# Kernel optimization log

Measured on AMD Instinct MI355X. Metric: run time of the kernel, lower is better.

The kernel has to match this reference:

```python
import jax, jax.numpy as jnp
import numpy as np

NV, NE, NT = 20000, 40000, 30000
D, H, L = 512, 8, 2
HD = D // H
SCALE = float(np.sqrt(HD))
EV, EE, ET = 160000, 160000, 120000
LN_EPS = 1e-5


def _layer_norm(x, g, b):
    m = jnp.mean(x, axis=-1, keepdims=True)
    v = jnp.mean((x - m) ** 2, axis=-1, keepdims=True)
    return (x - m) * jax.lax.rsqrt(v + LN_EPS) * g + b


def _attn_layer(x, ei, W, b, g, bt):
    # x: [N, D]; ei: [2, E]; W: [4, D, D] (q,k,v,out); b: [4, D]
    n = x.shape[0]
    resid = x
    q = (x @ W[0] + b[0]).reshape(n, H, HD)
    k = (x @ W[1] + b[1]).reshape(n, H, HD)
    v = (x @ W[2] + b[2]).reshape(n, H, HD)
    src, dst = ei[0], ei[1]
    # per-edge scores: query at target, key at source (k[edge_index[1]] gather in original)
    scores = jnp.sum(q[dst] * k[src], axis=-1) / SCALE        # [E, H]
    # NOTE: original applies softmax over dim=0, i.e. globally over the edge axis
    w = jax.nn.softmax(scores, axis=0)                         # [E, H]
    msgs = w[:, :, None] * v[src]                              # [E, H, HD]
    out = jax.ops.segment_sum(msgs, dst, num_segments=n)      # [N, H, HD]
    out = out.reshape(n, D) @ W[3] + b[3]
    return _layer_norm(out + resid, g, bt)


def _attn_stack(x, ei, W, b, g, bt):
    for l in range(L):
        x = _attn_layer(x, ei, W[l], b[l], g[l], bt[l])
    return x


def setup_inputs() -> dict:
    key = jax.random.key(0)
    ks = jax.random.split(key, 16)
    inp = {}
    inp['vertices'] = jax.random.normal(ks[0], (NV, D), jnp.float32)
    inp['edge_features'] = jax.random.normal(ks[1], (NE, D), jnp.float32)
    inp['triangle_features'] = jax.random.normal(ks[2], (NT, D), jnp.float32)
    inp['v_embed'] = jax.random.normal(ks[3], (NV, D), jnp.float32)
    inp['e_embed'] = jax.random.normal(ks[4], (NE, D), jnp.float32)
    inp['t_embed'] = jax.random.normal(ks[5], (NT, D), jnp.float32)
    inp['v_pos'] = jax.random.normal(ks[6], (NV, D), jnp.float32) * 0.1
    inp['e_pos'] = jax.random.normal(ks[7], (NE, D), jnp.float32) * 0.1
    inp['t_pos'] = jax.random.normal(ks[8], (NT, D), jnp.float32) * 0.1
    for name, k2 in (('v', ks[9]), ('e', ks[10]), ('t', ks[11])):
        inp[name + 'W'] = jax.random.normal(k2, (L, 4, D, D), jnp.float32) * 0.02
        inp[name + 'B'] = jnp.zeros((L, 4, D), jnp.float32)
        inp[name + 'G'] = jnp.ones((L, D), jnp.float32)
        inp[name + 'Bt'] = jnp.zeros((L, D), jnp.float32)
    inp['head_W'] = jax.random.normal(ks[12], (3, D, D), jnp.float32) * 0.02
    inp['head_b'] = jnp.zeros((3, D), jnp.float32)
    inp['v_ei'] = jax.random.randint(ks[13], (2, EV), 0, NV, jnp.int32)
    inp['e_ei'] = jax.random.randint(ks[14], (2, EE), 0, NE, jnp.int32)
    inp['t_ei'] = jax.random.randint(ks[15], (2, ET), 0, NT, jnp.int32)
    return inp


def reference(vertices, edge_features, triangle_features, v_embed, e_embed, t_embed,
              v_pos, e_pos, t_pos, vW, vB, vG, vBt, eW, eB, eG, eBt,
              tW, tB, tG, tBt, head_W, head_b, v_ei, e_ei, t_ei):
    # embedding(arange(N)) == full table lookup; add positional params and input features
    v = v_embed + v_pos + vertices
    e = e_embed + e_pos + edge_features
    t = t_embed + t_pos + triangle_features
    v = _attn_stack(v, v_ei, vW, vB, vG, vBt)
    e = _attn_stack(e, e_ei, eW, eB, eG, eBt)
    t = _attn_stack(t, t_ei, tW, tB, tG, tBt)
    v_out = v @ head_W[0] + head_b[0]
    e_out = e @ head_W[1] + head_b[1]
    t_out = t @ head_W[2] + head_b[2]
    return (v_out, e_out, t_out)
```

## Files before the change

### kernel.cpp

```cpp
#include <hip/hip_runtime.h>


typedef __attribute__((ext_vector_type(8))) __bf16 bf16x8;
typedef __attribute__((ext_vector_type(4))) float f32x4;
typedef __attribute__((ext_vector_type(8))) unsigned short ushort8v;
typedef __attribute__((ext_vector_type(4))) unsigned short ushort4v;

__device__ __forceinline__ float b2f(unsigned short u) {
  union { unsigned u; float f; } x; x.u = (unsigned)u << 16; return x.f;
}
__device__ __forceinline__ unsigned short f2b(float f) {
  union { float f; unsigned u; } x; x.f = f;
  unsigned r = x.u + 0x7fffu + ((x.u >> 16) & 1u);
  return (unsigned short)(r >> 16);
}
__device__ __forceinline__ int xcd_swizzle(int orig, int nwg) {
  const int xcd = orig & 7, lin = orig >> 3;
  const int q = nwg >> 3, r8 = nwg & 7;
  return (xcd < r8 ? xcd * (q + 1) : r8 * (q + 1) + (xcd - r8) * q) + lin;
}
__device__ __forceinline__ void stage16(const void* g, void* lds_uniform) {
  __builtin_amdgcn_global_load_lds(
      (const __attribute__((address_space(1))) void*)g,
      (__attribute__((address_space(3))) void*)lds_uniform, 16, 0, 0);
}

struct IB {
  const float4* a[3]; const float4* b[3]; const float4* c[3];
  unsigned short* xb[3];
  long long cum[4];
};
struct HB {
  const int* ei[3]; int E[3]; int cum[4];
  int* deg[3]; const int* rowptr[3]; int* srcs[3];
};
struct PB {
  const int* deg[3]; int* rowptr[3]; int N[3]; int nbcum[4];
};
struct GB {
  const unsigned short* A[3]; const unsigned short* BT[3];
  const float* bias[3]; void* C[3];
  int M[3]; int cum[4];
};
struct SB {
  const unsigned short* qkv[3]; const int* srcs[3]; const int* rowptr[3];
  float* sc[3]; float* pm[3]; float* ps[3];
  int N[3]; int cum[4];
};
struct MB {
  const float* pm[3]; const float* ps[3]; int nslots[3];
};
struct AB {
  const unsigned short* qkv[3]; const float* sc[3]; const int* srcs[3];
  const int* rowptr[3]; unsigned short* agg[3];
  int N[3]; int cum[4];
};
struct LB {
  const unsigned short* proj[3]; const float* g[3]; const float* bt[3];
  unsigned short* xb[3]; int N[3]; int cum[4];
};
__device__ __forceinline__ int find3(int b, const int* cum) {
  return (b >= cum[1]) + (b >= cum[2]);
}

__global__ __launch_bounds__(256) void init_b_kernel(IB ib)
{
  long long total = ib.cum[3];
  long long stride = (long long)gridDim.x * 256;
  for (long long i = (long long)blockIdx.x * 256 + threadIdx.x; i < total; i += stride) {
    int s = (i >= ib.cum[1]) + (i >= ib.cum[2]);
    long long j = i - ib.cum[s];
    float4 av = ib.a[s][j], bv = ib.b[s][j], cv = ib.c[s][j];
    ushort4v o;
    o.x = f2b(av.x + bv.x + cv.x); o.y = f2b(av.y + bv.y + cv.y);
    o.z = f2b(av.z + bv.z + cv.z); o.w = f2b(av.w + bv.w + cv.w);
    *(ushort4v*)(ib.xb[s] + j * 4) = o;
  }
}

__global__ __launch_bounds__(256) void transpose_all_kernel(
    const float* W0, const float* W1, const float* W2, const float* Wh,
    unsigned short* WT)
{
  __shared__ float t[32][33];
  int z = blockIdx.z;
  const float* src = (z < 8)  ? W0 + (size_t)z * 262144
                   : (z < 16) ? W1 + (size_t)(z - 8) * 262144
                   : (z < 24) ? W2 + (size_t)(z - 16) * 262144
                              : Wh + (size_t)(z - 24) * 262144;
  unsigned short* dst = WT + (size_t)z * 262144;
  int bx = blockIdx.x * 32, by = blockIdx.y * 32;
  int tx = threadIdx.x, ty = threadIdx.y;
  #pragma unroll
  for (int i = 0; i < 32; i += 8)
    t[ty + i][tx] = src[(size_t)(by + ty + i) * 512 + bx + tx];
  __syncthreads();
  #pragma unroll
  for (int i = 0; i < 32; i += 8) {
    int c = bx + ty + i;
    int p = (c & ~0x3C) | ((c & 0x30) >> 2) | ((c & 0x0C) << 2);
    dst[(size_t)p * 512 + by + tx] = f2b(t[tx][ty + i]);
  }
}

template<int OUT_BF16>
__global__ __launch_bounds__(512, 2) void gemm_big_kernel(GB gb, int Ncols)
{
  constexpr int K = 512;
  __shared__ unsigned short smem[81920];

  const int b = blockIdx.x;
  const int s = find3(b, gb.cum);
  const int wgid = xcd_swizzle(b - gb.cum[s], gb.cum[s + 1] - gb.cum[s]);
  const unsigned short* A  = gb.A[s];
  const unsigned short* BT = gb.BT[s];
  const float* bias = gb.bias[s];
  const int M = gb.M[s];

  const int tiles_n = Ncols >> 8;
  const int tm = wgid / tiles_n;
  const int tn = wgid - tm * tiles_n;
  const int row0 = tm << 8, col0 = tn << 8;
  const int lane = threadIdx.x & 63, wid = threadIdx.x >> 6;
  const int wr = (wid >> 2) << 7;
  const int wc = (wid & 3) << 6;

  f32x4 acc[8][4];
  #pragma unroll
  for (int i = 0; i < 8; ++i)
    #pragma unroll
    for (int j = 0; j < 4; ++j) acc[i][j] = (f32x4)0.f;

  int srow[4], scsw[4], sseg[4];
  #pragma unroll
  for (int i = 0; i < 4; ++i) {
    int seg = (i << 3) | wid;
    int idx = (seg << 6) | lane;
    int row = idx >> 3, ch = idx & 7;
    sseg[i] = seg; srow[i] = row; scsw[i] = ch ^ (row & 7);
  }

  #define STG_A(buf3, kb_, i)                                                 \
    { int ra = row0 + srow[i]; ra = (ra < M) ? ra : (M - 1);                  \
      stage16(A + (size_t)ra * K + (kb_) + (scsw[i] << 3),                    \
              smem + (buf3) * 16384 + (sseg[i] << 9)); }
  #define STG_B(buf2, kb_, i)                                                 \
    { int rb = col0 + srow[i];                                                \
      stage16(BT + (size_t)rb * K + (kb_) + (scsw[i] << 3),                   \
              smem + 49152 + (buf2) * 16384 + (sseg[i] << 9)); }

  STG_B(0, 0, 0) STG_B(0, 0, 1) STG_B(0, 0, 2) STG_B(0, 0, 3)
  STG_A(0, 0, 0) STG_A(0, 0, 1) STG_A(0, 0, 2) STG_A(0, 0, 3)
  STG_A(1, 64, 0) STG_A(1, 64, 1) STG_A(1, 64, 2) STG_A(1, 64, 3)
  asm volatile("s_waitcnt vmcnt(4)" ::: "memory");
  __builtin_amdgcn_s_barrier();

  const int lm = lane & 15;
  const int kbl = (lane >> 4) << 4;

  #pragma unroll
  for (int kt = 0; kt < 8; ++kt) {
    const char* Asb = (const char*)(smem + (kt % 3) * 16384);
    const char* Bsb = (const char*)(smem + 49152 + (kt & 1) * 16384);
    const int kb1 = (kt + 1) << 6, kb2 = (kt + 2) << 6;

    auto rdA = [&](int mi, int kk) -> bf16x8 {
      int r = wr + (mi << 4) + lm;
      int kb = (kk << 6) + kbl;
      return *(const bf16x8*)(Asb + (r << 7) + (kb ^ ((r & 7) << 4)));
    };
    auto rdB = [&](int ni, int kk) -> bf16x8 {
      int r = wc + (ni << 4) + lm;
      int kb = (kk << 6) + kbl;
      return *(const bf16x8*)(Bsb + (r << 7) + (kb ^ ((r & 7) << 4)));
    };

    bf16x8 av[4], bv[4];

    #pragma unroll
    for (int i = 0; i < 4; ++i) { av[i] = rdA(i, 0); bv[i] = rdB(i, 0); }
    if (kt < 7) {
      STG_B((kt + 1) & 1, kb1, 0) STG_B((kt + 1) & 1, kb1, 1)
      STG_B((kt + 1) & 1, kb1, 2) STG_B((kt + 1) & 1, kb1, 3)
    }
    __builtin_amdgcn_s_barrier();
    __builtin_amdgcn_s_setprio(1);
    #pragma unroll
    for (int mi = 0; mi < 4; ++mi)
      #pragma unroll
      for (int ni = 0; ni < 4; ++ni)
        acc[mi][ni] = __builtin_amdgcn_mfma_f32_16x16x32_bf16(
            bv[ni], av[mi], acc[mi][ni], 0, 0, 0);
    __builtin_amdgcn_s_setprio(0);
    __builtin_amdgcn_s_barrier();

    #pragma unroll
    for (int i = 0; i < 4; ++i) av[i] = rdA(4 + i, 0);
    if (kt < 6) {
      STG_A((kt + 2) % 3, kb2, 0) STG_A((kt + 2) % 3, kb2, 1)
      STG_A((kt + 2) % 3, kb2, 2) STG_A((kt + 2) % 3, kb2, 3)
    }
    __builtin_amdgcn_s_barrier();
    __builtin_amdgcn_s_setprio(1);
    #pragma unroll
    for (int mi = 0; mi < 4; ++mi)
      #pragma unroll
      for (int ni = 0; ni < 4; ++ni)
        acc[4 + mi][ni] = __builtin_amdgcn_mfma_f32_16x16x32_bf16(
            bv[ni], av[mi], acc[4 + mi][ni], 0, 0, 0);
    __builtin_amdgcn_s_setprio(0);
    __builtin_amdgcn_s_barrier();

    #pragma unroll
    for (int i = 0; i < 4; ++i) { av[i] = rdA(i, 1); bv[i] = rdB(i, 1); }
    __builtin_amdgcn_s_barrier();
    __builtin_amdgcn_s_setprio(1);
    #pragma unroll
    for (int mi = 0; mi < 4; ++mi)
      #pragma unroll
      for (int ni = 0; ni < 4; ++ni)
        acc[mi][ni] = __builtin_amdgcn_mfma_f32_16x16x32_bf16(
            bv[ni], av[mi], acc[mi][ni], 0, 0, 0);
    __builtin_amdgcn_s_setprio(0);
    __builtin_amdgcn_s_barrier();

    #pragma unroll
    for (int i = 0; i < 4; ++i) av[i] = rdA(4 + i, 1);
    __builtin_amdgcn_s_barrier();
    __builtin_amdgcn_s_setprio(1);
    #pragma unroll
    for (int mi = 0; mi < 4; ++mi)
      #pragma unroll
      for (int ni = 0; ni < 4; ++ni)
        acc[4 + mi][ni] = __builtin_amdgcn_mfma_f32_16x16x32_bf16(
            bv[ni], av[mi], acc[4 + mi][ni], 0, 0, 0);
    __builtin_amdgcn_s_setprio(0);

    if (kt < 6) {
      asm volatile("s_waitcnt vmcnt(4) lgkmcnt(0)" ::: "memory");
      __builtin_amdgcn_s_barrier();
    } else if (kt == 6) {
      asm volatile("s_waitcnt vmcnt(0) lgkmcnt(0)" ::: "memory");
      __builtin_amdgcn_s_barrier();
    }
  }
  #undef STG_A
  #undef STG_B

  const int mrow = lane & 15;
  const int t4 = (lane >> 4) << 4;
  float bsv[16];
  #pragma unroll
  for (int ni = 0; ni < 4; ++ni) {
    float4 bvv = *(const float4*)(bias + col0 + wc + t4 + (ni << 2));
    bsv[4*ni+0] = bvv.x; bsv[4*ni+1] = bvv.y; bsv[4*ni+2] = bvv.z; bsv[4*ni+3] = bvv.w;
  }

  if (OUT_BF16) {
    unsigned short* C = (unsigned short*)gb.C[s];
    #pragma unroll
    for (int mi = 0; mi < 8; ++mi) {
      int rowg = row0 + wr + (mi << 4) + mrow;
      if (rowg < M) {
        ushort8v o0, o1;
        #pragma unroll
        for (int r = 0; r < 4; ++r) {
          o0[r]     = f2b(acc[mi][0][r] + bsv[r]);
          o0[4 + r] = f2b(acc[mi][1][r] + bsv[4 + r]);
          o1[r]     = f2b(acc[mi][2][r] + bsv[8 + r]);
          o1[4 + r] = f2b(acc[mi][3][r] + bsv[12 + r]);
        }
        unsigned short* cp = C + (size_t)rowg * Ncols + col0 + wc + t4;
        *(ushort8v*)cp = o0;
        *(ushort8v*)(cp + 8) = o1;
      }
    }
  } else {
    float* C = (float*)gb.C[s];
    #pragma unroll
    for (int mi = 0; mi < 8; ++mi) {
      int rowg = row0 + wr + (mi << 4) + mrow;
      if (rowg < M) {
        float* cp = C + (size_t)rowg * Ncols + col0 + wc + t4;
        #pragma unroll
        for (int ni = 0; ni < 4; ++ni) {
          float4 v;
          v.x = acc[mi][ni][0] + bsv[4*ni+0];
          v.y = acc[mi][ni][1] + bsv[4*ni+1];
          v.z = acc[mi][ni][2] + bsv[4*ni+2];
          v.w = acc[mi][ni][3] + bsv[4*ni+3];
          *(float4*)(cp + (ni << 2)) = v;
        }
      }
    }
  }
}

template<int OUT_BF16>
__global__ __launch_bounds__(256) void gemm_sm_kernel(GB gb, int Ncols)
{
  constexpr int K = 512;
  __shared__ unsigned short As[8192];
  __shared__ unsigned short Bs[8192];

  const int b = blockIdx.x;
  const int s = find3(b, gb.cum);
  const int wgid = xcd_swizzle(b - gb.cum[s], gb.cum[s + 1] - gb.cum[s]);
  const unsigned short* A  = gb.A[s];
  const unsigned short* BT = gb.BT[s];
  const float* bias = gb.bias[s];
  const int M = gb.M[s];

  const int tiles_n = Ncols >> 7;
  const int tm = wgid / tiles_n;
  const int tn = wgid - tm * tiles_n;
  const int row0 = tm << 7, col0 = tn << 7;
  const int lane = threadIdx.x & 63, wid = threadIdx.x >> 6;
  const int wm = (wid >> 1) << 6, wn = (wid & 1) << 6;

  f32x4 acc[4][4];
  #pragma unroll
  for (int i = 0; i < 4; ++i)
    #pragma unroll
    for (int j = 0; j < 4; ++j) acc[i][j] = (f32x4)0.f;

  int srow[4], scsw[4], sseg[4];
  #pragma unroll
  for (int i = 0; i < 4; ++i) {
    int seg = (i << 2) | wid;
    int idx = (seg << 6) | lane;
    int row = idx >> 3, ch = idx & 7;
    sseg[i] = seg; srow[i] = row; scsw[i] = ch ^ (row & 7);
  }

  #pragma unroll
  for (int kt = 0; kt < 8; ++kt) {
    const int kbase = kt << 6;
    #pragma unroll
    for (int i = 0; i < 4; ++i) {
      int ra = row0 + srow[i]; ra = (ra < M) ? ra : (M - 1);
      stage16(A + (size_t)ra * K + kbase + (scsw[i] << 3), As + (sseg[i] << 9));
      int rb = col0 + srow[i];
      stage16(BT + (size_t)rb * K + kbase + (scsw[i] << 3), Bs + (sseg[i] << 9));
    }
    asm volatile("s_waitcnt vmcnt(0)" ::: "memory");
    __syncthreads();

    #pragma unroll
    for (int kk = 0; kk < 2; ++kk) {
      const int kb = (kk << 6) + ((lane >> 4) << 4);
      bf16x8 af[4], bfr[4];
      #pragma unroll
      for (int mi = 0; mi < 4; ++mi) {
        int r = wm + (mi << 4) + (lane & 15);
        af[mi] = *(const bf16x8*)((const char*)As + (r << 7) + (kb ^ ((r & 7) << 4)));
      }
      #pragma unroll
      for (int ni = 0; ni < 4; ++ni) {
        int r = wn + (ni << 4) + (lane & 15);
        bfr[ni] = *(const bf16x8*)((const char*)Bs + (r << 7) + (kb ^ ((r & 7) << 4)));
      }
      #pragma unroll
      for (int mi = 0; mi < 4; ++mi)
        #pragma unroll
        for (int ni = 0; ni < 4; ++ni)
          acc[mi][ni] = __builtin_amdgcn_mfma_f32_16x16x32_bf16(
              bfr[ni], af[mi], acc[mi][ni], 0, 0, 0);
    }
    __syncthreads();
  }

  const int mrow = lane & 15;
  const int t4 = (lane >> 4) << 4;
  float bsv[16];
  #pragma unroll
  for (int ni = 0; ni < 4; ++ni) {
    float4 bvv = *(const float4*)(bias + col0 + wn + t4 + (ni << 2));
    bsv[4*ni+0] = bvv.x; bsv[4*ni+1] = bvv.y; bsv[4*ni+2] = bvv.z; bsv[4*ni+3] = bvv.w;
  }

  if (OUT_BF16) {
    unsigned short* C = (unsigned short*)gb.C[s];
    #pragma unroll
    for (int mi = 0; mi < 4; ++mi) {
      int rowg = row0 + wm + (mi << 4) + mrow;
      if (rowg < M) {
        ushort8v o0, o1;
        #pragma unroll
        for (int r = 0; r < 4; ++r) {
          o0[r]     = f2b(acc[mi][0][r] + bsv[r]);
          o0[4 + r] = f2b(acc[mi][1][r] + bsv[4 + r]);
          o1[r]     = f2b(acc[mi][2][r] + bsv[8 + r]);
          o1[4 + r] = f2b(acc[mi][3][r] + bsv[12 + r]);
        }
        unsigned short* cp = C + (size_t)rowg * Ncols + col0 + wn + t4;
        *(ushort8v*)cp = o0;
        *(ushort8v*)(cp + 8) = o1;
      }
    }
  } else {
    float* C = (float*)gb.C[s];
    #pragma unroll
    for (int mi = 0; mi < 4; ++mi) {
      int rowg = row0 + wm + (mi << 4) + mrow;
      if (rowg < M) {
        float* cp = C + (size_t)rowg * Ncols + col0 + wn + t4;
        #pragma unroll
        for (int ni = 0; ni < 4; ++ni) {
          float4 v;
          v.x = acc[mi][ni][0] + bsv[4*ni+0];
          v.y = acc[mi][ni][1] + bsv[4*ni+1];
          v.z = acc[mi][ni][2] + bsv[4*ni+2];
          v.w = acc[mi][ni][3] + bsv[4*ni+3];
          *(float4*)(cp + (ni << 2)) = v;
        }
      }
    }
  }
}

__global__ __launch_bounds__(256) void scores_b_kernel(SB sb)
{
  int b = blockIdx.x;
  int s = find3(b, sb.cum);
  int lb = b - sb.cum[s];
  const unsigned short* qkv = sb.qkv[s];
  const int* srcs = sb.srcs[s];
  float* sc = sb.sc[s];
  int wid = threadIdx.x >> 6, lane = threadIdx.x & 63;
  int n = (lb << 2) | wid;
  float mx = -1e30f, sm = 0.f;
  if (n < sb.N[s]) {
    int beg = sb.rowptr[s][n], end = sb.rowptr[s][n + 1];
    if (beg < end) {
      ushort8v qv = *(const ushort8v*)(qkv + (size_t)n * 1536 + (lane << 3));
      float qf[8];
      #pragma unroll
      for (int j = 0; j < 8; ++j) qf[j] = b2f(qv[j]);
      int i = beg;
      for (; i + 2 <= end; i += 2) {
        int s0 = srcs[i], s1 = srcs[i + 1];
        ushort8v k0 = *(const ushort8v*)(qkv + (size_t)s0 * 1536 + 512 + (lane << 3));
        ushort8v k1 = *(const ushort8v*)(qkv + (size_t)s1 * 1536 + 512 + (lane << 3));
        float p0 = 0.f, p1 = 0.f;
        #pragma unroll
        for (int j = 0; j < 8; ++j) { p0 += qf[j] * b2f(k0[j]); p1 += qf[j] * b2f(k1[j]); }
        p0 += __shfl_xor(p0, 1); p1 += __shfl_xor(p1, 1);
        p0 += __shfl_xor(p0, 2); p1 += __shfl_xor(p1, 2);
        p0 += __shfl_xor(p0, 4); p1 += __shfl_xor(p1, 4);
        p0 *= 0.125f; p1 *= 0.125f;
        float nm = fmaxf(mx, fmaxf(p0, p1));
        sm = sm * __expf(mx - nm) + __expf(p0 - nm) + __expf(p1 - nm);
        mx = nm;
        if (!(lane & 7)) {
          sc[(size_t)i * 8 + (lane >> 3)] = p0;
          sc[(size_t)(i + 1) * 8 + (lane >> 3)] = p1;
        }
      }
      if (i < end) {
        int s0 = srcs[i];
        ushort8v k0 = *(const ushort8v*)(qkv + (size_t)s0 * 1536 + 512 + (lane << 3));
        float p0 = 0.f;
        #pragma unroll
        for (int j = 0; j < 8; ++j) p0 += qf[j] * b2f(k0[j]);
        p0 += __shfl_xor(p0, 1);
        p0 += __shfl_xor(p0, 2);
        p0 += __shfl_xor(p0, 4);
        p0 *= 0.125f;
        float nm = fmaxf(mx, p0);
        sm = sm * __expf(mx - nm) + __expf(p0 - nm);
        mx = nm;
        if (!(lane & 7)) sc[(size_t)i * 8 + (lane >> 3)] = p0;
      }
    }
  }
  if (!(lane & 7)) {
    size_t slot = ((size_t)lb << 2) | wid;
    sb.pm[s][slot * 8 + (lane >> 3)] = mx;
    sb.ps[s][slot * 8 + (lane >> 3)] = sm;
  }
}

__device__ __forceinline__ void pair_reduce_block(
    float (&m)[8], float (&s)[8], float* redm, float* reds)
{
  int lane = threadIdx.x & 63, wid = threadIdx.x >> 6;
  #pragma unroll
  for (int h = 0; h < 8; ++h)
    #pragma unroll
    for (int off = 1; off < 64; off <<= 1) {
      float om = __shfl_xor(m[h], off);
      float os = __shfl_xor(s[h], off);
      float M = fmaxf(m[h], om);
      s[h] = s[h] * __expf(m[h] - M) + os * __expf(om - M);
      m[h] = M;
    }
  if (lane == 0) {
    #pragma unroll
    for (int h = 0; h < 8; ++h) { redm[h * 4 + wid] = m[h]; reds[h * 4 + wid] = s[h]; }
  }
  __syncthreads();
  if (threadIdx.x == 0) {
    #pragma unroll
    for (int h = 0; h < 8; ++h) {
      float M = redm[h * 4], S = reds[h * 4];
      #pragma unroll
      for (int w = 1; w < 4; ++w) {
        float om = redm[h * 4 + w], os = reds[h * 4 + w];
        float nM = fmaxf(M, om);
        S = S * __expf(M - nM) + os * __expf(om - nM);
        M = nM;
      }
      m[h] = M; s[h] = S;
    }
  }
}

__global__ __launch_bounds__(256) void gms_part_b_kernel(
    MB mb, float* pm2, float* ps2)
{
  __shared__ float redm[32], reds[32];
  int s = blockIdx.x >> 8, j = blockIdx.x & 255;
  const float* pm = mb.pm[s];
  const float* ps = mb.ps[s];
  float m[8], sv[8];
  #pragma unroll
  for (int h = 0; h < 8; ++h) { m[h] = -1e30f; sv[h] = 0.f; }
  for (int i = j * 256 + threadIdx.x; i < mb.nslots[s]; i += 65536) {
    #pragma unroll
    for (int h = 0; h < 8; ++h) {
      float mi = pm[(size_t)i * 8 + h], si = ps[(size_t)i * 8 + h];
      float M = fmaxf(m[h], mi);
      sv[h] = sv[h] * __expf(m[h] - M) + si * __expf(mi - M);
      m[h] = M;
    }
  }
  pair_reduce_block(m, sv, redm, reds);
  if (threadIdx.x == 0) {
    #pragma unroll
    for (int h = 0; h < 8; ++h) {
      pm2[(s * 256 + j) * 8 + h] = m[h];
      ps2[(s * 256 + j) * 8 + h] = sv[h];
    }
  }
}

__global__ __launch_bounds__(256) void gms_final_b_kernel(
    const float* pm2, const float* ps2, float* gmax, float* ginv)
{
  __shared__ float redm[32], reds[32];
  int s = blockIdx.x;
  float m[8], sv[8];
  #pragma unroll
  for (int h = 0; h < 8; ++h) {
    m[h]  = pm2[(s * 256 + threadIdx.x) * 8 + h];
    sv[h] = ps2[(s * 256 + threadIdx.x) * 8 + h];
  }
  pair_reduce_block(m, sv, redm, reds);
  if (threadIdx.x == 0) {
    #pragma unroll
    for (int h = 0; h < 8; ++h) { gmax[s * 8 + h] = m[h]; ginv[s * 8 + h] = 1.0f / sv[h]; }
  }
}

__global__ __launch_bounds__(256) void hist_b_kernel(HB hb)
{
  int b = blockIdx.x;
  int s = find3(b, hb.cum);
  int e = (b - hb.cum[s]) * 256 + threadIdx.x;
  if (e < hb.E[s]) atomicAdd(&hb.deg[s][hb.ei[s][hb.E[s] + e]], 1);
}

__global__ __launch_bounds__(1024) void scan_part_b_kernel(PB pb, int* bsums)
{
  __shared__ int wsum[16];
  int b = blockIdx.x;
  int s = (b >= pb.nbcum[1]) + (b >= pb.nbcum[2]);
  int lb = b - pb.nbcum[s];
  int i = lb * 1024 + threadIdx.x;
  int lane = threadIdx.x & 63, wid = threadIdx.x >> 6;
  int sv = (i < pb.N[s]) ? pb.deg[s][i] : 0;
  #pragma unroll
  for (int off = 1; off < 64; off <<= 1) {
    int t = __shfl_up(sv, off);
    if (lane >= off) sv += t;
  }
  if (lane == 63) wsum[wid] = sv;
  __syncthreads();
  if (threadIdx.x < 16) {
    int ws = wsum[threadIdx.x];
    #pragma unroll
    for (int off = 1; off < 16; off <<= 1) {
      int t = __shfl_up(ws, off);
      if (threadIdx.x >= off) ws += t;
    }
    wsum[threadIdx.x] = ws;
  }
  __syncthreads();
  if (wid > 0) sv += wsum[wid - 1];
  if (i < pb.N[s]) pb.rowptr[s][i + 1] = sv;
  if (threadIdx.x == 1023) bsums[s * 64 + lb] = sv;
}

__global__ __launch_bounds__(64) void scan_bsums_b_kernel(
    int* bsums, int nb0, int nb1, int nb2)
{
  int s = blockIdx.x;
  int nb = (s == 0) ? nb0 : (s == 1) ? nb1 : nb2;
  int* bs = bsums + s * 64;
  int lane = threadIdx.x;
  int v = (lane < nb) ? bs[lane] : 0;
  #pragma unroll
  for (int off = 1; off < 64; off <<= 1) {
    int t = __shfl_up(v, off);
    if (lane >= off) v += t;
  }
  int ex = __shfl_up(v, 1);
  if (lane == 0) ex = 0;
  if (lane < nb) bs[lane] = ex;
}

__global__ __launch_bounds__(1024) void scan_add_b_kernel(
    PB pb, const int* bsums)
{
  int b = blockIdx.x;
  int s = (b >= pb.nbcum[1]) + (b >= pb.nbcum[2]);
  int lb = b - pb.nbcum[s];
  int i = lb * 1024 + threadIdx.x;
  if (lb == 0 && threadIdx.x == 0) pb.rowptr[s][0] = 0;
  if (i < pb.N[s] && lb > 0) pb.rowptr[s][i + 1] += bsums[s * 64 + lb];
}

__global__ __launch_bounds__(256) void scatter_b_kernel(HB hb)
{
  int b = blockIdx.x;
  int s = find3(b, hb.cum);
  int e = (b - hb.cum[s]) * 256 + threadIdx.x;
  if (e < hb.E[s]) {
    const int* ei = hb.ei[s];
    int dst = ei[hb.E[s] + e];
    int pos = atomicAdd(&hb.deg[s][dst], 1);
    hb.srcs[s][hb.rowptr[s][dst] + pos] = ei[e];
  }
}

__global__ __launch_bounds__(256) void aggregate_b_kernel(
    AB ab, const float* gmaxg, const float* ginvg)
{
  int b = blockIdx.x;
  int s = find3(b, ab.cum);
  int lb = b - ab.cum[s];
  int wid = threadIdx.x >> 6, lane = threadIdx.x & 63;
  int n = (lb << 2) | wid;
  if (n >= ab.N[s]) return;
  const unsigned short* qkv = ab.qkv[s];
  const float* sc = ab.sc[s];
  const int* srcs = ab.srcs[s];
  int beg = ab.rowptr[s][n], end = ab.rowptr[s][n + 1];
  int h = lane >> 3;
  float gm  = gmaxg[s * 8 + h];
  float inv = ginvg[s * 8 + h];
  float acc[8] = {0.f,0.f,0.f,0.f,0.f,0.f,0.f,0.f};
  int i = beg;
  for (; i + 4 <= end; i += 4) {
    int s0 = srcs[i], s1 = srcs[i + 1], s2 = srcs[i + 2], s3 = srcs[i + 3];
    float w0 = __expf(sc[(size_t)i * 8 + h] - gm) * inv;
    float w1 = __expf(sc[(size_t)(i + 1) * 8 + h] - gm) * inv;
    float w2 = __expf(sc[(size_t)(i + 2) * 8 + h] - gm) * inv;
    float w3 = __expf(sc[(size_t)(i + 3) * 8 + h] - gm) * inv;
    ushort8v v0 = *(const ushort8v*)(qkv + (size_t)s0 * 1536 + 1024 + (lane << 3));
    ushort8v v1 = *(const ushort8v*)(qkv + (size_t)s1 * 1536 + 1024 + (lane << 3));
    ushort8v v2 = *(const ushort8v*)(qkv + (size_t)s2 * 1536 + 1024 + (lane << 3));
    ushort8v v3 = *(const ushort8v*)(qkv + (size_t)s3 * 1536 + 1024 + (lane << 3));
    #pragma unroll
    for (int j = 0; j < 8; ++j)
      acc[j] += (w0 * b2f(v0[j]) + w1 * b2f(v1[j]))
              + (w2 * b2f(v2[j]) + w3 * b2f(v3[j]));
  }
  for (; i < end; ++i) {
    int s0 = srcs[i];
    float w0 = __expf(sc[(size_t)i * 8 + h] - gm) * inv;
    ushort8v v0 = *(const ushort8v*)(qkv + (size_t)s0 * 1536 + 1024 + (lane << 3));
    #pragma unroll
    for (int j = 0; j < 8; ++j) acc[j] += w0 * b2f(v0[j]);
  }
  ushort8v o;
  #pragma unroll
  for (int j = 0; j < 8; ++j) o[j] = f2b(acc[j]);
  *(ushort8v*)(ab.agg[s] + (size_t)n * 512 + (lane << 3)) = o;
}

__global__ __launch_bounds__(256) void ln_b_kernel(LB lb_)
{
  int b = blockIdx.x;
  int s = find3(b, lb_.cum);
  int lb = b - lb_.cum[s];
  int wid = threadIdx.x >> 6, lane = threadIdx.x & 63;
  int n = (lb << 2) | wid;
  if (n >= lb_.N[s]) return;
  size_t base = (size_t)n * 512 + (lane << 3);
  ushort8v pv = *(const ushort8v*)(lb_.proj[s] + base);
  ushort8v xv = *(const ushort8v*)(lb_.xb[s] + base);
  float y[8];
  #pragma unroll
  for (int j = 0; j < 8; ++j) y[j] = b2f(pv[j]) + b2f(xv[j]);
  float sum = 0.f;
  #pragma unroll
  for (int j = 0; j < 8; ++j) sum += y[j];
  #pragma unroll
  for (int off = 1; off < 64; off <<= 1) sum += __shfl_xor(sum, off);
  float mean = sum * (1.f / 512.f);
  float vs = 0.f;
  #pragma unroll
  for (int j = 0; j < 8; ++j) { float d = y[j] - mean; vs += d * d; }
  #pragma unroll
  for (int off = 1; off < 64; off <<= 1) vs += __shfl_xor(vs, off);
  float rstd = rsqrtf(vs * (1.f / 512.f) + 1e-5f);
  int gi = lane << 3;
  ushort8v ob;
  #pragma unroll
  for (int j = 0; j < 8; ++j)
    ob[j] = f2b((y[j] - mean) * rstd * lb_.g[s][gi + j] + lb_.bt[s][gi + j]);
  *(ushort8v*)(lb_.xb[s] + base) = ob;
}

extern "C" void kernel_launch(void* const* d_in, const int* in_sizes, int n_in,
                              void* d_out, int out_size, void* d_ws, size_t ws_size,
                              hipStream_t stream)
{
  (void)n_in; (void)out_size;
  const float* feat[3] = {(const float*)d_in[0], (const float*)d_in[1], (const float*)d_in[2]};
  const float* emb[3]  = {(const float*)d_in[3], (const float*)d_in[4], (const float*)d_in[5]};
  const float* pos[3]  = {(const float*)d_in[6], (const float*)d_in[7], (const float*)d_in[8]};
  const float* W[3]  = {(const float*)d_in[9],  (const float*)d_in[13], (const float*)d_in[17]};
  const float* Bb[3] = {(const float*)d_in[10], (const float*)d_in[14], (const float*)d_in[18]};
  const float* G[3]  = {(const float*)d_in[11], (const float*)d_in[15], (const float*)d_in[19]};
  const float* Bt[3] = {(const float*)d_in[12], (const float*)d_in[16], (const float*)d_in[20]};
  const float* headW = (const float*)d_in[21];
  const float* headB = (const float*)d_in[22];
  const int* ei[3] = {(const int*)d_in[23], (const int*)d_in[24], (const int*)d_in[25]};

  int Ns[3], Es[3];
  for (int s = 0; s < 3; ++s) { Ns[s] = in_sizes[s] / 512; Es[s] = in_sizes[23 + s] / 2; }

  long long Noff[4] = {0}, Eoff[4] = {0}, Roff[4] = {0}, Poff[4] = {0};
  for (int s = 0; s < 3; ++s) {
    Noff[s + 1] = Noff[s] + Ns[s];
    Eoff[s + 1] = Eoff[s] + Es[s];
    Roff[s + 1] = Roff[s] + Ns[s] + 1;
    Poff[s + 1] = Poff[s] + ((Ns[s] + 3) / 4) * 4;
  }

  char* base = (char*)d_ws;
  size_t off = 0;
  auto carve = [&](size_t bytes) -> char* {
    char* r = base + off;
    off += (bytes + 255) & ~(size_t)255;
    return r;
  };
  unsigned short* WT   = (unsigned short*)carve((size_t)27 * 262144 * 2);
  unsigned short* XB   = (unsigned short*)carve((size_t)Noff[3] * 512 * 2);
  unsigned short* QKV  = (unsigned short*)carve((size_t)Noff[3] * 1536 * 2);
  float*          SC   = (float*)carve((size_t)Eoff[3] * 8 * 4);
  unsigned short* AGG  = (unsigned short*)carve((size_t)Noff[3] * 512 * 2);
  int*   ROWPTR = (int*)carve((size_t)Roff[3] * 4);
  int*   DEG    = (int*)carve((size_t)Noff[3] * 4);
  int*   SRCS   = (int*)carve((size_t)Eoff[3] * 4);
  int*   BSUMS  = (int*)carve(3 * 64 * 4);
  float* PARTM  = (float*)carve((size_t)Poff[3] * 8 * 4);
  float* PARTS1 = (float*)carve((size_t)Poff[3] * 8 * 4);
  float* PARTM2 = (float*)carve(3 * 256 * 8 * 4);
  float* PARTS2 = (float*)carve(3 * 256 * 8 * 4);
  float* GMAX   = (float*)carve(256);
  float* GINV   = (float*)carve(256);
  if (off > ws_size) return;

  unsigned short* XBs[3];  unsigned short* QKVs[3]; float* SCs[3];
  unsigned short* AGGs[3]; int* ROWPTRs[3]; int* DEGs[3]; int* SRCSs[3];
  float* PMs[3]; float* PSs[3];
  for (int s = 0; s < 3; ++s) {
    XBs[s]  = XB  + Noff[s] * 512;
    QKVs[s] = QKV + Noff[s] * 1536;
    SCs[s]  = SC  + Eoff[s] * 8;
    AGGs[s] = AGG + Noff[s] * 512;
    ROWPTRs[s] = ROWPTR + Roff[s];
    DEGs[s] = DEG + Noff[s];
    SRCSs[s] = SRCS + Eoff[s];
    PMs[s] = PARTM + Poff[s] * 8;
    PSs[s] = PARTS1 + Poff[s] * 8;
  }

  transpose_all_kernel<<<dim3(16, 16, 27), dim3(32, 8), 0, stream>>>(
      W[0], W[1], W[2], headW, WT);

  IB ib;
  for (int s = 0; s < 3; ++s) {
    ib.a[s] = (const float4*)feat[s]; ib.b[s] = (const float4*)emb[s];
    ib.c[s] = (const float4*)pos[s];  ib.xb[s] = XBs[s];
  }
  ib.cum[0] = 0;
  for (int s = 0; s < 3; ++s) ib.cum[s + 1] = ib.cum[s] + (long long)Ns[s] * 128;
  init_b_kernel<<<2048, 256, 0, stream>>>(ib);

  HB hb;
  hb.cum[0] = 0;
  for (int s = 0; s < 3; ++s) {
    hb.ei[s] = ei[s]; hb.E[s] = Es[s];
    hb.cum[s + 1] = hb.cum[s] + (Es[s] + 255) / 256;
    hb.deg[s] = DEGs[s]; hb.rowptr[s] = ROWPTRs[s]; hb.srcs[s] = SRCSs[s];
  }
  PB pb;
  pb.nbcum[0] = 0;
  for (int s = 0; s < 3; ++s) {
    pb.deg[s] = DEGs[s]; pb.rowptr[s] = ROWPTRs[s]; pb.N[s] = Ns[s];
    pb.nbcum[s + 1] = pb.nbcum[s] + (Ns[s] + 1023) / 1024;
  }
  hipMemsetAsync(DEG, 0, (size_t)Noff[3] * 4, stream);
  hist_b_kernel<<<hb.cum[3], 256, 0, stream>>>(hb);
  scan_part_b_kernel<<<pb.nbcum[3], 1024, 0, stream>>>(pb, BSUMS);
  scan_bsums_b_kernel<<<3, 64, 0, stream>>>(
      BSUMS, (Ns[0] + 1023) / 1024, (Ns[1] + 1023) / 1024, (Ns[2] + 1023) / 1024);
  scan_add_b_kernel<<<pb.nbcum[3], 1024, 0, stream>>>(pb, BSUMS);
  hipMemsetAsync(DEG, 0, (size_t)Noff[3] * 4, stream);
  scatter_b_kernel<<<hb.cum[3], 256, 0, stream>>>(hb);

  int nsbcum[4] = {0}, mtcum[4] = {0}, mtscum[4] = {0};
  for (int s = 0; s < 3; ++s) {
    nsbcum[s + 1] = nsbcum[s] + (Ns[s] + 3) / 4;
    mtcum[s + 1]  = mtcum[s]  + ((Ns[s] + 255) >> 8) * 6;
    mtscum[s + 1] = mtscum[s] + ((Ns[s] + 127) >> 7) * 4;
  }

  MB mb;
  for (int s = 0; s < 3; ++s) {
    mb.pm[s] = PMs[s]; mb.ps[s] = PSs[s];
    mb.nslots[s] = ((Ns[s] + 3) / 4) * 4;
  }

  for (int l = 0; l < 2; ++l) {
    GB qg;
    for (int s = 0; s < 3; ++s) {
      qg.A[s] = XBs[s];
      qg.BT[s] = WT + (size_t)(s * 8 + l * 4) * 262144;
      qg.bias[s] = Bb[s] + (size_t)l * 2048;
      qg.C[s] = QKVs[s];
      qg.M[s] = Ns[s];
      qg.cum[s] = mtcum[s];
    }
    qg.cum[3] = mtcum[3];
    gemm_big_kernel<1><<<mtcum[3], 512, 0, stream>>>(qg, 1536);

    SB sb;
    for (int s = 0; s < 3; ++s) {
      sb.qkv[s] = QKVs[s]; sb.srcs[s] = SRCSs[s]; sb.rowptr[s] = ROWPTRs[s];
      sb.sc[s] = SCs[s]; sb.pm[s] = PMs[s]; sb.ps[s] = PSs[s];
      sb.N[s] = Ns[s]; sb.cum[s] = nsbcum[s];
    }
    sb.cum[3] = nsbcum[3];
    scores_b_kernel<<<nsbcum[3], 256, 0, stream>>>(sb);

    gms_part_b_kernel<<<768, 256, 0, stream>>>(mb, PARTM2, PARTS2);
    gms_final_b_kernel<<<3, 256, 0, stream>>>(PARTM2, PARTS2, GMAX, GINV);

    AB ab;
    for (int s = 0; s < 3; ++s) {
      ab.qkv[s] = QKVs[s]; ab.sc[s] = SCs[s]; ab.srcs[s] = SRCSs[s];
      ab.rowptr[s] = ROWPTRs[s]; ab.agg[s] = AGGs[s];
      ab.N[s] = Ns[s]; ab.cum[s] = nsbcum[s];
    }
    ab.cum[3] = nsbcum[3];
    aggregate_b_kernel<<<nsbcum[3], 256, 0, stream>>>(ab, GMAX, GINV);

    GB pg;
    for (int s = 0; s < 3; ++s) {
      pg.A[s] = AGGs[s];
      pg.BT[s] = WT + (size_t)(s * 8 + l * 4 + 3) * 262144;
      pg.bias[s] = Bb[s] + (size_t)(l * 2048 + 1536);
      pg.C[s] = QKVs[s];
      pg.M[s] = Ns[s];
      pg.cum[s] = mtscum[s];
    }
    pg.cum[3] = mtscum[3];
    gemm_sm_kernel<1><<<mtscum[3], 256, 0, stream>>>(pg, 512);

    LB lb;
    for (int s = 0; s < 3; ++s) {
      lb.proj[s] = QKVs[s]; lb.g[s] = G[s] + (size_t)l * 512;
      lb.bt[s] = Bt[s] + (size_t)l * 512; lb.xb[s] = XBs[s];
      lb.N[s] = Ns[s]; lb.cum[s] = nsbcum[s];
    }
    lb.cum[3] = nsbcum[3];
    ln_b_kernel<<<nsbcum[3], 256, 0, stream>>>(lb);
  }

  GB hg;
  size_t out_off = 0;
  for (int s = 0; s < 3; ++s) {
    hg.A[s] = XBs[s];
    hg.BT[s] = WT + (size_t)(24 + s) * 262144;
    hg.bias[s] = headB + (size_t)s * 512;
    hg.C[s] = (float*)d_out + out_off;
    hg.M[s] = Ns[s];
    hg.cum[s] = mtscum[s];
    out_off += (size_t)Ns[s] * 512;
  }
  hg.cum[3] = mtscum[3];
  gemm_sm_kernel<0><<<mtscum[3], 256, 0, stream>>>(hg, 512);
}
```

Before: 1.206 ms.

## Double-buffer LDS staging in small GEMM and drop intra-iteration barriers

The small GEMM kernel now uses two LDS buffers and prefetches the next K-tile with global_load_lds while running MFMAs on the current one, so load latency overlaps with compute. The large GEMM kernel's per-phase s_barrier pairs around each MFMA cluster are removed, leaving only the end-of-iteration waitcnt plus barrier. This lowers synchronization stalls but loosens wave lockstep, which may change how LDS reads and staging writes interleave. Double buffering doubles the small GEMM's LDS footprint to 64 KB, which may reduce occupancy.

```diff
diff --git a/kernel.cpp b/kernel.cpp
--- a/kernel.cpp
+++ b/kernel.cpp
@@ -183,7 +183,6 @@
       STG_B((kt + 1) & 1, kb1, 0) STG_B((kt + 1) & 1, kb1, 1)
       STG_B((kt + 1) & 1, kb1, 2) STG_B((kt + 1) & 1, kb1, 3)
     }
-    __builtin_amdgcn_s_barrier();
     __builtin_amdgcn_s_setprio(1);
     #pragma unroll
     for (int mi = 0; mi < 4; ++mi)
@@ -192,7 +191,6 @@
         acc[mi][ni] = __builtin_amdgcn_mfma_f32_16x16x32_bf16(
             bv[ni], av[mi], acc[mi][ni], 0, 0, 0);
     __builtin_amdgcn_s_setprio(0);
-    __builtin_amdgcn_s_barrier();
 
     #pragma unroll
     for (int i = 0; i < 4; ++i) av[i] = rdA(4 + i, 0);
@@ -200,7 +198,6 @@
       STG_A((kt + 2) % 3, kb2, 0) STG_A((kt + 2) % 3, kb2, 1)
       STG_A((kt + 2) % 3, kb2, 2) STG_A((kt + 2) % 3, kb2, 3)
     }
-    __builtin_amdgcn_s_barrier();
     __builtin_amdgcn_s_setprio(1);
     #pragma unroll
     for (int mi = 0; mi < 4; ++mi)
@@ -209,11 +206,9 @@
         acc[4 + mi][ni] = __builtin_amdgcn_mfma_f32_16x16x32_bf16(
             bv[ni], av[mi], acc[4 + mi][ni], 0, 0, 0);
     __builtin_amdgcn_s_setprio(0);
-    __builtin_amdgcn_s_barrier();
 
     #pragma unroll
     for (int i = 0; i < 4; ++i) { av[i] = rdA(i, 1); bv[i] = rdB(i, 1); }
-    __builtin_amdgcn_s_barrier();
     __builtin_amdgcn_s_setprio(1);
     #pragma unroll
     for (int mi = 0; mi < 4; ++mi)
@@ -222,11 +217,9 @@
         acc[mi][ni] = __builtin_amdgcn_mfma_f32_16x16x32_bf16(
             bv[ni], av[mi], acc[mi][ni], 0, 0, 0);
     __builtin_amdgcn_s_setprio(0);
-    __builtin_amdgcn_s_barrier();
 
     #pragma unroll
     for (int i = 0; i < 4; ++i) av[i] = rdA(4 + i, 1);
-    __builtin_amdgcn_s_barrier();
     __builtin_amdgcn_s_setprio(1);
     #pragma unroll
     for (int mi = 0; mi < 4; ++mi)
@@ -300,8 +293,7 @@
 __global__ __launch_bounds__(256) void gemm_sm_kernel(GB gb, int Ncols)
 {
   constexpr int K = 512;
-  __shared__ unsigned short As[8192];
-  __shared__ unsigned short Bs[8192];
+  __shared__ unsigned short smem[32768];
 
   const int b = blockIdx.x;
   const int s = find3(b, gb.cum);
@@ -333,19 +325,29 @@
     sseg[i] = seg; srow[i] = row; scsw[i] = ch ^ (row & 7);
   }
 
+  #define STAGE_SM(buf, kb_)                                                  \
+    _Pragma("unroll")                                                         \
+    for (int i = 0; i < 4; ++i) {                                             \
+      int ra = row0 + srow[i]; ra = (ra < M) ? ra : (M - 1);                  \
+      stage16(A + (size_t)ra * K + (kb_) + (scsw[i] << 3),                    \
+              smem + (buf) * 16384 + (sseg[i] << 9));                         \
+      int rb = col0 + srow[i];                                                \
+      stage16(BT + (size_t)rb * K + (kb_) + (scsw[i] << 3),                   \
+              smem + (buf) * 16384 + 8192 + (sseg[i] << 9));                  \
+    }
+
+  STAGE_SM(0, 0)
+  asm volatile("s_waitcnt vmcnt(0)" ::: "memory");
+  __syncthreads();
+
   #pragma unroll
   for (int kt = 0; kt < 8; ++kt) {
-    const int kbase = kt << 6;
-    #pragma unroll
-    for (int i = 0; i < 4; ++i) {
-      int ra = row0 + srow[i]; ra = (ra < M) ? ra : (M - 1);
-      stage16(A + (size_t)ra * K + kbase + (scsw[i] << 3), As + (sseg[i] << 9));
-      int rb = col0 + srow[i];
-      stage16(BT + (size_t)rb * K + kbase + (scsw[i] << 3), Bs + (sseg[i] << 9));
-    }
-    asm volatile("s_waitcnt vmcnt(0)" ::: "memory");
-    __syncthreads();
-
+    const int cur = kt & 1;
+    if (kt < 7) {
+      STAGE_SM(cur ^ 1, (kt + 1) << 6)
+    }
+    const unsigned short* As = smem + cur * 16384;
+    const unsigned short* Bs = As + 8192;
     #pragma unroll
     for (int kk = 0; kk < 2; ++kk) {
       const int kb = (kk << 6) + ((lane >> 4) << 4);
@@ -367,8 +369,10 @@
           acc[mi][ni] = __builtin_amdgcn_mfma_f32_16x16x32_bf16(
               bfr[ni], af[mi], acc[mi][ni], 0, 0, 0);
     }
+    asm volatile("s_waitcnt vmcnt(0)" ::: "memory");
     __syncthreads();
   }
+  #undef STAGE_SM
 
   const int mrow = lane & 15;
   const int t4 = (lane >> 4) << 4;
```

After: 1.214 ms. Within noise of the previous version (+0.6%).
